# Performance work log

Measured on AMD Instinct MI355X. Metric: run time of the kernel, lower is better.

The kernel has to match this reference:

```python
import jax, jax.numpy as jnp
import numpy as np

EPS = 1e-10


def setup_inputs() -> dict:
    key = jax.random.key(0)
    k_logits, k_temp, k_exp = jax.random.split(key, 3)
    B, V = 256, 128000
    logits = jax.random.normal(k_logits, (B, V), dtype=jnp.float32)
    temperatures = jax.random.uniform(k_temp, (B,), dtype=jnp.float32, minval=0.1, maxval=2.0)
    # first quarter of rows are greedy (temperature == 0), as in the torch.where branch
    temperatures = temperatures.at[: B // 4].set(0.0)
    # single exponential(1) noise row of shape (vocab,), expanded across batch in the kernel
    exponential = jax.random.exponential(k_exp, (V,), dtype=jnp.float32)
    return {"logits": logits, "temperatures": temperatures, "exponential": exponential}


def reference(logits, temperatures, exponential):
    # logits: [B, V] fp32, temperatures: [B], exponential: [V] shared across rows
    logits = logits.astype(jnp.float32)
    greedy = temperatures == 0.0                      # [B]
    safe_t = jnp.where(greedy, 1.0, temperatures)      # avoid div-by-zero on greedy rows
    # temperature-scaled softmax, single stable pass
    probs = jax.nn.softmax(logits / safe_t[:, None], axis=-1)  # [B, V]
    # Gumbel-max via exponential noise: argmax(p / E) ~ Categorical(p)
    noisy = probs / (exponential[None, :] + EPS)       # [B, V]
    scores = jnp.where(greedy[:, None], logits, noisy) # greedy rows: raw argmax
    sampled_tokens = jnp.argmax(scores, axis=-1).astype(jnp.int32)  # [B]
    return sampled_tokens
```

## Files before the change

### kernel.cpp

```cpp
#include <hip/hip_runtime.h>
#include <hip/hip_bf16.h>
#include <math.h>

#define EPS 1e-10f

__global__ __launch_bounds__(256) void logE_kernel(const float* __restrict__ e,
                                                   float* __restrict__ logE,
                                                   int V) {
    int i = blockIdx.x * blockDim.x + threadIdx.x;
    if (i < V) logE[i] = logf(e[i] + EPS);
}

template <bool PRECOMP>
__global__ __launch_bounds__(1024) void sampler_kernel(const float* __restrict__ logits,
                                                       const float* __restrict__ temps,
                                                       const float* __restrict__ noise,
                                                       int* __restrict__ out,
                                                       int V) {
    const int row = blockIdx.x;
    const float t = temps[row];
    const bool greedy = (t == 0.0f);
    const float inv_t = greedy ? 1.0f : (1.0f / t);

    const float4* rl4 = reinterpret_cast<const float4*>(logits + (size_t)row * (size_t)V);
    const float4* n4  = reinterpret_cast<const float4*>(noise);

    float best = -INFINITY;
    int   bidx = 0x7fffffff;

    const int nvec = V >> 2;

    if (greedy) {
        for (int i = threadIdx.x; i < nvec; i += blockDim.x) {
            float4 l = rl4[i];
            int base = i << 2;
            if (l.x > best) { best = l.x; bidx = base;     }
            if (l.y > best) { best = l.y; bidx = base + 1; }
            if (l.z > best) { best = l.z; bidx = base + 2; }
            if (l.w > best) { best = l.w; bidx = base + 3; }
        }
    } else {
        for (int i = threadIdx.x; i < nvec; i += blockDim.x) {
            float4 l = rl4[i];
            float4 g = n4[i];
            float g0, g1, g2, g3;
            if (PRECOMP) {
                g0 = g.x; g1 = g.y; g2 = g.z; g3 = g.w;
            } else {
                g0 = logf(g.x + EPS); g1 = logf(g.y + EPS);
                g2 = logf(g.z + EPS); g3 = logf(g.w + EPS);
            }
            float s0 = fmaf(l.x, inv_t, -g0);
            float s1 = fmaf(l.y, inv_t, -g1);
            float s2 = fmaf(l.z, inv_t, -g2);
            float s3 = fmaf(l.w, inv_t, -g3);
            int base = i << 2;
            if (s0 > best) { best = s0; bidx = base;     }
            if (s1 > best) { best = s1; bidx = base + 1; }
            if (s2 > best) { best = s2; bidx = base + 2; }
            if (s3 > best) { best = s3; bidx = base + 3; }
        }
    }

    #pragma unroll
    for (int off = 32; off >= 1; off >>= 1) {
        float ov = __shfl_down(best, off);
        int   oi = __shfl_down(bidx, off);
        if (ov > best || (ov == best && oi < bidx)) { best = ov; bidx = oi; }
    }

    __shared__ float sv[16];
    __shared__ int   si[16];
    const int wid  = threadIdx.x >> 6;
    const int lane = threadIdx.x & 63;
    const int nw   = blockDim.x >> 6;
    if (lane == 0) { sv[wid] = best; si[wid] = bidx; }
    __syncthreads();

    if (wid == 0) {
        best = (lane < nw) ? sv[lane] : -INFINITY;
        bidx = (lane < nw) ? si[lane] : 0x7fffffff;
        #pragma unroll
        for (int off = 8; off >= 1; off >>= 1) {
            float ov = __shfl_down(best, off);
            int   oi = __shfl_down(bidx, off);
            if (ov > best || (ov == best && oi < bidx)) { best = ov; bidx = oi; }
        }
        if (lane == 0) out[row] = bidx;
    }
}

extern "C" void kernel_launch(void* const* d_in, const int* in_sizes, int n_in,
                              void* d_out, int out_size, void* d_ws, size_t ws_size,
                              hipStream_t stream) {
    const float* logits = (const float*)d_in[0];
    const float* temps  = (const float*)d_in[1];
    const float* expo   = (const float*)d_in[2];
    int*         out    = (int*)d_out;

    const int B = in_sizes[1];
    const int V = in_sizes[2];

    if (ws_size >= (size_t)V * sizeof(float)) {
        float* logE = (float*)d_ws;
        logE_kernel<<<(V + 255) / 256, 256, 0, stream>>>(expo, logE, V);
        sampler_kernel<true><<<B, 1024, 0, stream>>>(logits, temps, logE, out, V);
    } else {
        sampler_kernel<false><<<B, 1024, 0, stream>>>(logits, temps, expo, out, V);
    }
}
```

Before: 30.62 us.

## Split each row into segments with two-stage argmax and inline log noise

```diff
diff --git a/kernel.cpp b/kernel.cpp
--- a/kernel.cpp
+++ b/kernel.cpp
@@ -4,35 +4,38 @@
 
 #define EPS 1e-10f
 
-__global__ __launch_bounds__(256) void logE_kernel(const float* __restrict__ e,
-                                                   float* __restrict__ logE,
-                                                   int V) {
-    int i = blockIdx.x * blockDim.x + threadIdx.x;
-    if (i < V) logE[i] = logf(e[i] + EPS);
-}
+typedef float floatx4 __attribute__((ext_vector_type(4)));
 
-template <bool PRECOMP>
-__global__ __launch_bounds__(1024) void sampler_kernel(const float* __restrict__ logits,
-                                                       const float* __restrict__ temps,
-                                                       const float* __restrict__ noise,
-                                                       int* __restrict__ out,
-                                                       int V) {
-    const int row = blockIdx.x;
+__global__ __launch_bounds__(256) void partial_argmax_kernel(
+    const float* __restrict__ logits,
+    const float* __restrict__ temps,
+    const float* __restrict__ expo,
+    float* __restrict__ pv,
+    int*   __restrict__ pi,
+    int B, int V, int segLen) {
+
+    const int bid = blockIdx.x;
+    const int row = bid % B;
+    const int seg = bid / B;
+
     const float t = temps[row];
     const bool greedy = (t == 0.0f);
     const float inv_t = greedy ? 1.0f : (1.0f / t);
 
-    const float4* rl4 = reinterpret_cast<const float4*>(logits + (size_t)row * (size_t)V);
-    const float4* n4  = reinterpret_cast<const float4*>(noise);
+    const int beg4 = (seg * segLen) >> 2;
+    int end4 = ((seg + 1) * segLen) >> 2;
+    const int v4 = V >> 2;
+    if (end4 > v4) end4 = v4;
+
+    const floatx4* rl4 = reinterpret_cast<const floatx4*>(logits + (size_t)row * (size_t)V);
+    const floatx4* e4  = reinterpret_cast<const floatx4*>(expo);
 
     float best = -INFINITY;
     int   bidx = 0x7fffffff;
 
-    const int nvec = V >> 2;
-
     if (greedy) {
-        for (int i = threadIdx.x; i < nvec; i += blockDim.x) {
-            float4 l = rl4[i];
+        for (int i = beg4 + threadIdx.x; i < end4; i += 256) {
+            floatx4 l = __builtin_nontemporal_load(&rl4[i]);
             int base = i << 2;
             if (l.x > best) { best = l.x; bidx = base;     }
             if (l.y > best) { best = l.y; bidx = base + 1; }
@@ -40,20 +43,13 @@
             if (l.w > best) { best = l.w; bidx = base + 3; }
         }
     } else {
-        for (int i = threadIdx.x; i < nvec; i += blockDim.x) {
-            float4 l = rl4[i];
-            float4 g = n4[i];
-            float g0, g1, g2, g3;
-            if (PRECOMP) {
-                g0 = g.x; g1 = g.y; g2 = g.z; g3 = g.w;
-            } else {
-                g0 = logf(g.x + EPS); g1 = logf(g.y + EPS);
-                g2 = logf(g.z + EPS); g3 = logf(g.w + EPS);
-            }
-            float s0 = fmaf(l.x, inv_t, -g0);
-            float s1 = fmaf(l.y, inv_t, -g1);
-            float s2 = fmaf(l.z, inv_t, -g2);
-            float s3 = fmaf(l.w, inv_t, -g3);
+        for (int i = beg4 + threadIdx.x; i < end4; i += 256) {
+            floatx4 l = __builtin_nontemporal_load(&rl4[i]);
+            floatx4 g = e4[i];
+            float s0 = fmaf(l.x, inv_t, -logf(g.x + EPS));
+            float s1 = fmaf(l.y, inv_t, -logf(g.y + EPS));
+            float s2 = fmaf(l.z, inv_t, -logf(g.z + EPS));
+            float s3 = fmaf(l.w, inv_t, -logf(g.w + EPS));
             int base = i << 2;
             if (s0 > best) { best = s0; bidx = base;     }
             if (s1 > best) { best = s1; bidx = base + 1; }
@@ -69,14 +65,82 @@
         if (ov > best || (ov == best && oi < bidx)) { best = ov; bidx = oi; }
     }
 
-    __shared__ float sv[16];
-    __shared__ int   si[16];
+    __shared__ float sv[4];
+    __shared__ int   si[4];
     const int wid  = threadIdx.x >> 6;
     const int lane = threadIdx.x & 63;
-    const int nw   = blockDim.x >> 6;
     if (lane == 0) { sv[wid] = best; si[wid] = bidx; }
     __syncthreads();
 
+    if (threadIdx.x == 0) {
+        best = sv[0]; bidx = si[0];
+        #pragma unroll
+        for (int w = 1; w < 4; ++w) {
+            if (sv[w] > best || (sv[w] == best && si[w] < bidx)) { best = sv[w]; bidx = si[w]; }
+        }
+        pv[bid] = best;
+        pi[bid] = bidx;
+    }
+}
+
+__global__ __launch_bounds__(256) void final_reduce_kernel(
+    const float* __restrict__ pv,
+    const int*   __restrict__ pi,
+    int* __restrict__ out,
+    int B, int S) {
+    const int r = threadIdx.x;
+    if (r >= B) return;
+    float best = pv[r];
+    int   bidx = pi[r];
+    for (int s = 1; s < S; ++s) {
+        float v = pv[s * B + r];
+        int   i = pi[s * B + r];
+        if (v > best) { best = v; bidx = i; }
+    }
+    out[r] = bidx;
+}
+
+__global__ __launch_bounds__(1024) void row_argmax_kernel(
+    const float* __restrict__ logits,
+    const float* __restrict__ temps,
+    const float* __restrict__ expo,
+    int* __restrict__ out, int V) {
+    const int row = blockIdx.x;
+    const float t = temps[row];
+    const bool greedy = (t == 0.0f);
+    const float inv_t = greedy ? 1.0f : (1.0f / t);
+    const floatx4* rl4 = reinterpret_cast<const floatx4*>(logits + (size_t)row * (size_t)V);
+    const floatx4* e4  = reinterpret_cast<const floatx4*>(expo);
+    float best = -INFINITY; int bidx = 0x7fffffff;
+    const int nvec = V >> 2;
+    for (int i = threadIdx.x; i < nvec; i += blockDim.x) {
+        floatx4 l = rl4[i];
+        float s0, s1, s2, s3;
+        if (greedy) { s0 = l.x; s1 = l.y; s2 = l.z; s3 = l.w; }
+        else {
+            floatx4 g = e4[i];
+            s0 = fmaf(l.x, inv_t, -logf(g.x + EPS));
+            s1 = fmaf(l.y, inv_t, -logf(g.y + EPS));
+            s2 = fmaf(l.z, inv_t, -logf(g.z + EPS));
+            s3 = fmaf(l.w, inv_t, -logf(g.w + EPS));
+        }
+        int base = i << 2;
+        if (s0 > best) { best = s0; bidx = base;     }
+        if (s1 > best) { best = s1; bidx = base + 1; }
+        if (s2 > best) { best = s2; bidx = base + 2; }
+        if (s3 > best) { best = s3; bidx = base + 3; }
+    }
+    #pragma unroll
+    for (int off = 32; off >= 1; off >>= 1) {
+        float ov = __shfl_down(best, off);
+        int   oi = __shfl_down(bidx, off);
+        if (ov > best || (ov == best && oi < bidx)) { best = ov; bidx = oi; }
+    }
+    __shared__ float sv[16];
+    __shared__ int   si[16];
+    const int wid = threadIdx.x >> 6, lane = threadIdx.x & 63, nw = blockDim.x >> 6;
+    if (lane == 0) { sv[wid] = best; si[wid] = bidx; }
+    __syncthreads();
     if (wid == 0) {
         best = (lane < nw) ? sv[lane] : -INFINITY;
         bidx = (lane < nw) ? si[lane] : 0x7fffffff;
@@ -101,11 +165,16 @@
     const int B = in_sizes[1];
     const int V = in_sizes[2];
 
-    if (ws_size >= (size_t)V * sizeof(float)) {
-        float* logE = (float*)d_ws;
-        logE_kernel<<<(V + 255) / 256, 256, 0, stream>>>(expo, logE, V);
-        sampler_kernel<true><<<B, 1024, 0, stream>>>(logits, temps, logE, out, V);
+    const int S = 8;
+    const int segLen = ((V + S - 1) / S + 3) & ~3;
+    const size_t need = (size_t)S * B * (sizeof(float) + sizeof(int));
+
+    if (ws_size >= need) {
+        float* pv = (float*)d_ws;
+        int*   pi = (int*)(pv + (size_t)S * B);
+        partial_argmax_kernel<<<S * B, 256, 0, stream>>>(logits, temps, expo, pv, pi, B, V, segLen);
+        final_reduce_kernel<<<1, 256, 0, stream>>>(pv, pi, out, B, S);
     } else {
-        sampler_kernel<false><<<B, 1024, 0, stream>>>(logits, temps, expo, out, V);
+        row_argmax_kernel<<<B, 1024, 0, stream>>>(logits, temps, expo, out, V);
     }
 }
```

Result: slower. 33.17 us (+8.3%).
